# Kernel optimization log

Hardware: AMD Instinct MI355X
Metric: run time of the kernel (lower is better)

The kernel has to match this reference:

```python
import jax, jax.numpy as jnp
import numpy as np

N = 50000
E = 800000
HIGH, LOW, EMB = 128, 32, 64
HID, HEADS, OUT = 32, 8, 8
IN1 = HIGH + EMB  # 192
IN2 = HID * HEADS  # 256
NEG_SLOPE = 0.2


def setup_inputs() -> dict:
    key = jax.random.key(0)
    ks = jax.random.split(key, 12)
    s = lambda k, shape: (jax.random.normal(k, shape, dtype=jnp.float32) * 0.1)
    return {
        "high_dim_features": jax.random.normal(ks[0], (N, HIGH), dtype=jnp.float32),
        "low_dim_features": jax.random.normal(ks[1], (N, LOW), dtype=jnp.float32),
        "edge_index": jax.random.randint(ks[2], (2, E), 0, N, dtype=jnp.int32),
        "W_emb": s(ks[3], (LOW, EMB)),
        "b_emb": jnp.zeros((EMB,), jnp.float32),
        "W1": s(ks[4], (IN1, HEADS * HID)),
        "att_src1": s(ks[5], (HEADS, HID)),
        "att_dst1": s(ks[6], (HEADS, HID)),
        "b1": jnp.zeros((HEADS * HID,), jnp.float32),
        "W2": s(ks[7], (IN2, OUT)),
        "att_src2": s(ks[8], (1, OUT)),
        "att_dst2": s(ks[9], (1, OUT)),
        "b2": jnp.zeros((OUT,), jnp.float32),
    }


def _gat_layer(x, src, dst, W, att_src, att_dst, bias, heads, out_ch, concat):
    # x: [N, F_in]; src/dst: [E'] (self-loops already appended)
    n = x.shape[0]
    h = (x @ W).reshape(n, heads, out_ch)            # [N, H, C]
    a_src = jnp.einsum('nhc,hc->nh', h, att_src)     # [N, H]
    a_dst = jnp.einsum('nhc,hc->nh', h, att_dst)
    alpha = a_src[src] + a_dst[dst]                  # [E', H]
    alpha = jax.nn.leaky_relu(alpha, NEG_SLOPE)
    # segment softmax over incoming edges per destination node
    m = jax.ops.segment_max(alpha, dst, num_segments=n)
    ea = jnp.exp(alpha - m[dst])
    z = jax.ops.segment_sum(ea, dst, num_segments=n)
    alpha = ea / (z[dst] + 1e-16)                    # [E', H]
    msg = h[src] * alpha[:, :, None]                 # [E', H, C]
    out = jax.ops.segment_sum(msg, dst, num_segments=n)  # [N, H, C]
    if concat:
        out = out.reshape(n, heads * out_ch)
    else:
        out = out.mean(axis=1)
    return out + bias


def reference(high_dim_features, low_dim_features, edge_index,
              W_emb, b_emb, W1, att_src1, att_dst1, b1,
              W2, att_src2, att_dst2, b2):
    # embedding + elu, concat
    emb = jax.nn.elu(low_dim_features @ W_emb + b_emb)
    x = jnp.concatenate([high_dim_features, emb], axis=1)  # [N, IN1]
    # add self-loops (PyG default)
    loops = jnp.arange(N, dtype=edge_index.dtype)
    src = jnp.concatenate([edge_index[0], loops])
    dst = jnp.concatenate([edge_index[1], loops])
    x = _gat_layer(x, src, dst, W1, att_src1, att_dst1, b1, HEADS, HID, True)
    x = jax.nn.elu(x)  # dropout: eval mode no-op
    x = _gat_layer(x, src, dst, W2, att_src2, att_dst2, b2, 1, OUT, False)
    return jax.nn.log_softmax(x, axis=1)
```

## Files before the change

kernel.cpp:

```cpp
#include <hip/hip_runtime.h>
#include <hip/hip_bf16.h>

typedef __hip_bfloat16 bf16;
typedef short bf16x8 __attribute__((ext_vector_type(8)));
typedef float f32x4  __attribute__((ext_vector_type(4)));

#define CHK 2048

__device__ __forceinline__ float bf2f(bf16 v){ return __bfloat162float(v); }
__device__ __forceinline__ bf16  f2bf(float f){ return __float2bfloat16(f); }
__device__ __forceinline__ float lrelu(float a){ return a > 0.f ? a : 0.2f*a; }
__device__ __forceinline__ float bfbits(short s){
    union{unsigned u; float f;} cv; cv.u = ((unsigned)(unsigned short)s) << 16; return cv.f;
}
__device__ __forceinline__ short bf16s(float f){ bf16 q = f2bf(f); return *(short*)&q; }
__device__ __forceinline__ float cvtf(const void* p, int i, int isb){
    return isb ? bf2f(((const bf16*)p)[i]) : ((const float*)p)[i];
}
__device__ __forceinline__ short cvts(const void* p, int i, int isb){
    return isb ? ((const short*)p)[i] : bf16s(((const float*)p)[i]);
}
__device__ __forceinline__ bf16x8 load8(const void* base, size_t off, int isb){
    if (isb) return *(const bf16x8*)((const bf16*)base + off);
    const float* f = (const float*)base + off;
    f32x4 v0 = *(const f32x4*)f;
    f32x4 v1 = *(const f32x4*)(f + 4);
    short r[8];
    #pragma unroll
    for (int j = 0; j < 4; j++) r[j]   = bf16s(v0[j]);
    #pragma unroll
    for (int j = 0; j < 4; j++) r[4+j] = bf16s(v1[j]);
    return *(const bf16x8*)r;
}

__global__ __launch_bounds__(256) void k_init(const unsigned short* __restrict__ raw,
        int* __restrict__ flag, const int* __restrict__ dst,
        int* __restrict__ bucketCnt, int E, int NBUK, int nBlk){
    __shared__ int h[256];
    int t = threadIdx.x;
    if (blockIdx.x == 0){
        unsigned short w = raw[2*t];
        int e = (w >> 7) & 0xFF;
        int ok = (e >= 90 && e <= 140) ? 1 : 0;
        __shared__ int cnt;
        if (t == 0) cnt = 0;
        __syncthreads();
        atomicAdd(&cnt, ok);
        __syncthreads();
        if (t == 0) *flag = (cnt >= 192) ? 1 : 0;
    }
    h[t] = 0;
    __syncthreads();
    for (int i = blockIdx.x*256 + t; i < E; i += nBlk*256)
        atomicAdd(&h[((unsigned)dst[i]) >> 8], 1);
    __syncthreads();
    if (t < NBUK && h[t]) atomicAdd(&bucketCnt[t], h[t]);
}

__global__ __launch_bounds__(256) void k_prep(const void* __restrict__ low,
        const void* __restrict__ Wemb, const void* __restrict__ bemb,
        const void* __restrict__ W1, const void* __restrict__ W2,
        bf16* __restrict__ emb, bf16* __restrict__ Bp, bf16* __restrict__ Bp2,
        const int* __restrict__ flag, int N, int nEmb){
    __shared__ float wem[2048 + 64];
    __shared__ short lows[1024];
    int t = threadIdx.x;
    int b = blockIdx.x;
    int isb = *flag;
    if (b >= nEmb){
        int i = (b - nEmb)*256 + t;
        if (i < 16*6*64*8){
            int j = i & 7;
            int lane = (i >> 3) & 63;
            int r = i >> 9;
            int kt = r % 6, nt = r / 6;
            int k = kt*32 + (lane >> 4)*8 + j;
            int n = nt*16 + (lane & 15);
            *(short*)&Bp[i] = cvts(W1, k*256 + n, isb);
        } else {
            int i2 = i - 16*6*64*8;
            if (i2 >= 8*64*8) return;
            int j = i2 & 7;
            int lane = (i2 >> 3) & 63;
            int kt = i2 >> 9;
            int k = kt*32 + (lane >> 4)*8 + j;
            int n = lane & 15;
            *(short*)&Bp2[i2] = (n < 8) ? cvts(W2, k*8 + n, isb) : (short)0;
        }
        return;
    }
    for (int i = t; i < 2048; i += 256) wem[i] = cvtf(Wemb, i, isb);
    if (t < 64) wem[2048 + t] = cvtf(bemb, t, isb);
    int nl = t >> 3, j8 = (t & 7) * 8;
    for (int tile = 0; tile < 4; tile++){
        int nb0 = b*128 + tile*32;
        __syncthreads();
        int lim = (N - nb0) * 32;
        if (lim > 1024) lim = 1024;
        if (lim < 0) lim = 0;
        for (int i = t; i < 1024; i += 256)
            lows[i] = (i < lim) ? cvts(low, nb0*32 + i, isb) : (short)0;
        __syncthreads();
        float acc[8];
        #pragma unroll
        for (int j = 0; j < 8; j++) acc[j] = wem[2048 + j8 + j];
        for (int k = 0; k < 32; k++){
            float lv = bfbits(lows[nl*32 + k]);
            f32x4 w0 = *(const f32x4*)&wem[k*64 + j8];
            f32x4 w1 = *(const f32x4*)&wem[k*64 + j8 + 4];
            #pragma unroll
            for (int j = 0; j < 4; j++) acc[j]   += lv * w0[j];
            #pragma unroll
            for (int j = 0; j < 4; j++) acc[4+j] += lv * w1[j];
        }
        int n = nb0 + nl;
        if (n < N){
            short ov[8];
            #pragma unroll
            for (int j = 0; j < 8; j++){
                float v = acc[j];
                ov[j] = bf16s(v > 0.f ? v : expm1f(v));
            }
            *(bf16x8*)&emb[(size_t)n*64 + j8] = *(const bf16x8*)ov;
        }
    }
}

__global__ __launch_bounds__(256) void k_bscan(const int* __restrict__ bucketCnt,
        int* __restrict__ bucketPtr, int* __restrict__ bucketCur,
        int* __restrict__ rowptr, int N, int E, int NBUK){
    __shared__ int sd[256];
    int t = threadIdx.x;
    int v = (t < NBUK) ? bucketCnt[t] : 0;
    sd[t] = v;
    __syncthreads();
    #pragma unroll
    for (int off = 1; off < 256; off <<= 1){
        int a = (t >= off) ? sd[t - off] : 0;
        __syncthreads();
        sd[t] += a;
        __syncthreads();
    }
    int excl = sd[t] - v;
    if (t < NBUK){ bucketPtr[t] = excl; bucketCur[t*16] = excl; }
    if (t == 0){ bucketPtr[NBUK] = sd[255]; rowptr[N] = E + N; }
}

__global__ __launch_bounds__(256) void k_sg(
        const int* __restrict__ ei, int* __restrict__ bucketCur, int* __restrict__ pk,
        const void* __restrict__ highv, const bf16* __restrict__ emb,
        const bf16* __restrict__ Bp, const void* __restrict__ attS,
        const void* __restrict__ attD, bf16* __restrict__ h1,
        float* __restrict__ a_s, float* __restrict__ a_d,
        const int* __restrict__ flag, int N, int E, int nScat, int NBUK){
    const int RS = 260;
    __shared__ union SM {
        struct { short Ah[64*128]; short Ae[64*64]; } a;
        struct { float eb[16*260 + 16]; } g;
        struct { unsigned short dstS[CHK]; int hist[4][256]; int cur[4][256]; } s;
    } sm;
    __shared__ float att[512];
    int t = threadIdx.x;
    if ((int)blockIdx.x < nScat){
        int base = blockIdx.x * CHK;
        int cnt = E - base; if (cnt > CHK) cnt = CHK;
        int wv = t >> 6, lane = t & 63;
        #pragma unroll
        for (int w = 0; w < 4; w++) sm.s.hist[w][t] = 0;
        __syncthreads();
        const int* dstp = ei + E + base;
        const int* srcp = ei + base;
        int per = (cnt + 3) >> 2;
        int wb = wv*per, we = wb + per;
        if (we > cnt) we = cnt;
        if (wb > cnt) wb = cnt;
        for (int i = wb + lane; i < we; i += 64){
            int d = dstp[i];
            sm.s.dstS[i] = (unsigned short)d;
            atomicAdd(&sm.s.hist[wv][((unsigned)d) >> 8], 1);
        }
        __syncthreads();
        if (t < NBUK){
            int h0 = sm.s.hist[0][t], h1v = sm.s.hist[1][t];
            int h2 = sm.s.hist[2][t], h3 = sm.s.hist[3][t];
            int c = h0 + h1v + h2 + h3;
            int bs = c ? atomicAdd(&bucketCur[t*16], c) : 0;
            sm.s.cur[0][t] = bs;
            sm.s.cur[1][t] = bs + h0;
            sm.s.cur[2][t] = bs + h0 + h1v;
            sm.s.cur[3][t] = bs + h0 + h1v + h2;
        }
        __syncthreads();
        for (int i = wb + lane; i < we; i += 64){
            int d = sm.s.dstS[i];
            int pos = atomicAdd(&sm.s.cur[wv][d >> 8], 1);
            pk[pos] = ((d & 255) << 24) | srcp[i];
        }
        return;
    }
    int isb = *flag;
    att[t] = cvtf(attS, t, isb);
    att[256 + t] = cvtf(attD, t, isb);
    int w = t >> 6, lane = t & 63;
    int m_lo = lane & 15, quad = lane >> 4;
    int m0 = (blockIdx.x - nScat) * 64;

    #pragma unroll
    for (int ii = 0; ii < 4; ii++){
        int id = t + ii*256;
        int r = id >> 4, c = id & 15;
        int gr = m0 + r; if (gr >= N) gr = N-1;
        bf16x8 v = load8(highv, (size_t)gr*128 + c*8, isb);
        *(bf16x8*)&sm.a.Ah[r*128 + ((c ^ (r & 7)) << 3)] = v;
    }
    #pragma unroll
    for (int ii = 0; ii < 2; ii++){
        int id = t + ii*256;
        int r = id >> 3, c = id & 7;
        int gr = m0 + r; if (gr >= N) gr = N-1;
        bf16x8 v = *(const bf16x8*)&emb[(size_t)gr*64 + c*8];
        *(bf16x8*)&sm.a.Ae[r*64 + ((c ^ (r & 7)) << 3)] = v;
    }
    __syncthreads();

    f32x4 acc[4][4];
    #pragma unroll
    for (int rt = 0; rt < 4; rt++)
        #pragma unroll
        for (int ct = 0; ct < 4; ct++) acc[rt][ct] = (f32x4){0.f,0.f,0.f,0.f};

    int sw = m_lo & 7;
    #pragma unroll 2
    for (int kt = 0; kt < 6; kt++){
        bf16x8 a[4], b[4];
        if (kt < 4){
            int ch = (kt*4 + quad) ^ sw;
            #pragma unroll
            for (int rt = 0; rt < 4; rt++)
                a[rt] = *(const bf16x8*)&sm.a.Ah[(rt*16 + m_lo)*128 + (ch << 3)];
        } else {
            int ch = ((kt-4)*4 + quad) ^ sw;
            #pragma unroll
            for (int rt = 0; rt < 4; rt++)
                a[rt] = *(const bf16x8*)&sm.a.Ae[(rt*16 + m_lo)*64 + (ch << 3)];
        }
        #pragma unroll
        for (int ct = 0; ct < 4; ct++)
            b[ct] = *(const bf16x8*)&Bp[(size_t)(((w*4 + ct)*6 + kt)*64 + lane)*8];
        #pragma unroll
        for (int rt = 0; rt < 4; rt++)
            #pragma unroll
            for (int ct = 0; ct < 4; ct++)
                acc[rt][ct] = __builtin_amdgcn_mfma_f32_16x16x32_bf16(a[rt], b[ct], acc[rt][ct], 0, 0, 0);
    }

    float* eb = sm.g.eb;
    #pragma unroll 1
    for (int rt = 0; rt < 4; rt++){
        __syncthreads();
        #pragma unroll
        for (int ct = 0; ct < 4; ct++)
            #pragma unroll
            for (int reg = 0; reg < 4; reg++)
                eb[(quad*4 + reg)*RS + w*64 + ct*16 + m_lo] = acc[rt][ct][reg];
        __syncthreads();
        int r = t >> 4, cb = t & 15;
        int c0 = cb * 16;
        int m = m0 + rt*16 + r;
        f32x4 v[4];
        #pragma unroll
        for (int p = 0; p < 4; p++) v[p] = *(const f32x4*)&eb[r*RS + c0 + p*4];
        float ps = 0.f, pd = 0.f;
        #pragma unroll
        for (int p = 0; p < 4; p++)
            #pragma unroll
            for (int j = 0; j < 4; j++){
                ps += v[p][j] * att[c0 + p*4 + j];
                pd += v[p][j] * att[256 + c0 + p*4 + j];
            }
        if (m < N){
            short ov[16];
            #pragma unroll
            for (int p = 0; p < 4; p++)
                #pragma unroll
                for (int j = 0; j < 4; j++) ov[p*4+j] = bf16s(v[p][j]);
            *(bf16x8*)&h1[(size_t)m*256 + c0]     = *(const bf16x8*)&ov[0];
            *(bf16x8*)&h1[(size_t)m*256 + c0 + 8] = *(const bf16x8*)&ov[8];
        }
        ps += __shfl_xor(ps, 1);
        pd += __shfl_xor(pd, 1);
        if (((t & 1) == 0) && m < N){
            int hd = cb >> 1;
            a_s[m*8 + hd] = ps;
            a_d[m*8 + hd] = pd;
        }
    }
}

__global__ __launch_bounds__(256) void k_fine(const int* __restrict__ bucketPtr,
        const int* __restrict__ pk, int* __restrict__ rowptr, int* __restrict__ srcs,
        int N){
    __shared__ int hist[4][256];
    __shared__ int cur[4][256];
    __shared__ int sd[256];
    int t = threadIdx.x;
    int wv = t >> 6, lane = t & 63;
    int b = blockIdx.x;
    int d0 = b << 8;
    int nd = N - d0; if (nd > 256) nd = 256; if (nd < 0) nd = 0;
    int ebeg = bucketPtr[b], eend = bucketPtr[b+1];
    int tot = eend - ebeg;
    int per = (tot + 3) >> 2;
    int wb = wv*per, we = wb + per;
    if (we > tot) we = tot;
    if (wb > tot) wb = tot;
    #pragma unroll
    for (int w = 0; w < 4; w++) hist[w][t] = 0;
    __syncthreads();
    for (int i = wb + lane; i < we; i += 64)
        atomicAdd(&hist[wv][((unsigned)pk[ebeg + i]) >> 24], 1);
    __syncthreads();
    int h0 = hist[0][t], h1 = hist[1][t], h2 = hist[2][t], h3 = hist[3][t];
    int selfc = (t < nd) ? 1 : 0;
    int v = selfc + h0 + h1 + h2 + h3;
    sd[t] = v;
    __syncthreads();
    #pragma unroll
    for (int off = 1; off < 256; off <<= 1){
        int a = (t >= off) ? sd[t - off] : 0;
        __syncthreads();
        sd[t] += a;
        __syncthreads();
    }
    int r = ebeg + d0 + sd[t] - v;
    if (t < nd){
        rowptr[d0 + t] = r;
        srcs[r] = d0 + t;
    }
    int c0 = r + selfc;
    cur[0][t] = c0;
    cur[1][t] = c0 + h0;
    cur[2][t] = c0 + h0 + h1;
    cur[3][t] = c0 + h0 + h1 + h2;
    __syncthreads();
    for (int i = wb + lane; i < we; i += 64){
        int p = pk[ebeg + i];
        int pos = atomicAdd(&cur[wv][((unsigned)p) >> 24], 1);
        srcs[pos] = p & 0xFFFFFF;
    }
}

__global__ __launch_bounds__(256) void k_edge1(const int* __restrict__ rowptr,
        const int* __restrict__ srcs, const float* __restrict__ a_s,
        const float* __restrict__ a_d, const bf16* __restrict__ h1,
        const void* __restrict__ b1, bf16* __restrict__ x2,
        const int* __restrict__ flag, int N){
    int t = threadIdx.x;
    int lane = t & 63, wv = t >> 6;
    int n = blockIdx.x*4 + wv;
    if (n >= N) return;
    int beg = rowptr[n];
    int deg = rowptr[n+1] - beg;

    int cl = lane & 31;
    int hb = cl >> 2;
    int half = lane >> 5;
    float adb = a_d[n*8 + hb];

    float acc[8];
    #pragma unroll
    for (int j = 0; j < 8; j++) acc[j] = 0.f;
    float z = 0.f;

    int e = half;
    for (; e + 6 < deg; e += 8){
        int s0 = srcs[beg + e];
        int s1 = srcs[beg + e + 2];
        int s2 = srcs[beg + e + 4];
        int s3 = srcs[beg + e + 6];
        float w0 = __expf(fminf(lrelu(a_s[s0*8 + hb] + adb), 80.f));
        float w1 = __expf(fminf(lrelu(a_s[s1*8 + hb] + adb), 80.f));
        float w2 = __expf(fminf(lrelu(a_s[s2*8 + hb] + adb), 80.f));
        float w3 = __expf(fminf(lrelu(a_s[s3*8 + hb] + adb), 80.f));
        bf16x8 v0 = *(const bf16x8*)&h1[(size_t)s0*256 + cl*8];
        bf16x8 v1 = *(const bf16x8*)&h1[(size_t)s1*256 + cl*8];
        bf16x8 v2 = *(const bf16x8*)&h1[(size_t)s2*256 + cl*8];
        bf16x8 v3 = *(const bf16x8*)&h1[(size_t)s3*256 + cl*8];
        z += (w0 + w1) + (w2 + w3);
        #pragma unroll
        for (int j = 0; j < 8; j++) acc[j] += w0 * bfbits(v0[j]);
        #pragma unroll
        for (int j = 0; j < 8; j++) acc[j] += w1 * bfbits(v1[j]);
        #pragma unroll
        for (int j = 0; j < 8; j++) acc[j] += w2 * bfbits(v2[j]);
        #pragma unroll
        for (int j = 0; j < 8; j++) acc[j] += w3 * bfbits(v3[j]);
    }
    for (; e < deg; e += 2){
        int s = srcs[beg + e];
        float w = __expf(fminf(lrelu(a_s[s*8 + hb] + adb), 80.f));
        bf16x8 hv = *(const bf16x8*)&h1[(size_t)s*256 + cl*8];
        z += w;
        #pragma unroll
        for (int j = 0; j < 8; j++) acc[j] += w * bfbits(hv[j]);
    }
    #pragma unroll
    for (int j = 0; j < 8; j++) acc[j] += __shfl_xor(acc[j], 32);
    z += __shfl_xor(z, 32);
    float rz = 1.f / (z + 1e-16f);

    if (half == 0){
        int isb = *flag;
        bf16x8 bv = load8(b1, cl*8, isb);
        short ov[8];
        #pragma unroll
        for (int j = 0; j < 8; j++){
            float v = acc[j] * rz + bfbits(bv[j]);
            ov[j] = bf16s(v > 0.f ? v : expm1f(v));
        }
        *(bf16x8*)&x2[(size_t)n*256 + cl*8] = *(const bf16x8*)ov;
    }
}

__global__ __launch_bounds__(256) void k_gemm2(const bf16* __restrict__ x2,
        const bf16* __restrict__ Bp2, const void* __restrict__ attS,
        const void* __restrict__ attD, float* __restrict__ h2,
        float* __restrict__ a2s, float* __restrict__ a2d,
        const int* __restrict__ flag, int N){
    int t = threadIdx.x;
    int isb = *flag;
    int w = t >> 6, lane = t & 63;
    int m_lo = lane & 15, quad = lane >> 4;
    int m0 = blockIdx.x*64 + w*16;
    int mr = m0 + m_lo; if (mr >= N) mr = N-1;
    f32x4 acc = (f32x4){0.f,0.f,0.f,0.f};
    #pragma unroll
    for (int kt = 0; kt < 8; kt++){
        bf16x8 a = *(const bf16x8*)&x2[(size_t)mr*256 + kt*32 + quad*8];
        bf16x8 b = *(const bf16x8*)&Bp2[(size_t)(kt*64 + lane)*8];
        acc = __builtin_amdgcn_mfma_f32_16x16x32_bf16(a, b, acc, 0, 0, 0);
    }
    float s2 = (m_lo < 8) ? cvtf(attS, m_lo, isb) : 0.f;
    float d2 = (m_lo < 8) ? cvtf(attD, m_lo, isb) : 0.f;
    #pragma unroll
    for (int reg = 0; reg < 4; reg++){
        int m = m0 + quad*4 + reg;
        float val = acc[reg];
        float ps = val * s2, pd = val * d2;
        ps += __shfl_xor(ps, 1); ps += __shfl_xor(ps, 2);
        ps += __shfl_xor(ps, 4); ps += __shfl_xor(ps, 8);
        pd += __shfl_xor(pd, 1); pd += __shfl_xor(pd, 2);
        pd += __shfl_xor(pd, 4); pd += __shfl_xor(pd, 8);
        if (m < N){
            if (m_lo < 8) h2[(size_t)m*8 + m_lo] = val;
            if (m_lo == 0){ a2s[m] = ps; a2d[m] = pd; }
        }
    }
}

__global__ __launch_bounds__(256) void k_edge2(const int* __restrict__ rowptr,
        const int* __restrict__ srcs, const float* __restrict__ a2s,
        const float* __restrict__ a2d, const float* __restrict__ h2,
        const void* __restrict__ b2, void* __restrict__ outv,
        const int* __restrict__ flag, int N){
    int t = threadIdx.x;
    int lane = t & 63, wv = t >> 6;
    int n = blockIdx.x*4 + wv;
    if (n >= N) return;
    int beg = rowptr[n];
    int deg = rowptr[n+1] - beg;
    float adh = a2d[n];
    int ep = lane >> 3, c = lane & 7;
    float acc = 0.f, z = 0.f;
    for (int e = ep; e < deg; e += 8){
        int s = srcs[beg + e];
        float w = __expf(fminf(lrelu(a2s[s] + adh), 80.f));
        z += w;
        acc += w * h2[(size_t)s*8 + c];
    }
    acc += __shfl_xor(acc, 8);
    acc += __shfl_xor(acc, 16);
    acc += __shfl_xor(acc, 32);
    z += __shfl_xor(z, 8);
    z += __shfl_xor(z, 16);
    z += __shfl_xor(z, 32);
    int isb = *flag;
    float val = acc / (z + 1e-16f) + cvtf(b2, c, isb);
    float mx = val;
    mx = fmaxf(mx, __shfl_xor(mx, 1));
    mx = fmaxf(mx, __shfl_xor(mx, 2));
    mx = fmaxf(mx, __shfl_xor(mx, 4));
    float se = __expf(val - mx);
    se += __shfl_xor(se, 1); se += __shfl_xor(se, 2); se += __shfl_xor(se, 4);
    float r = val - mx - __logf(se);
    if (lane < 8){
        if (isb) ((bf16*)outv)[(size_t)n*8 + c] = f2bf(r);
        else     ((float*)outv)[(size_t)n*8 + c] = r;
    }
}

extern "C" void kernel_launch(void* const* d_in, const int* in_sizes, int n_in,
                              void* d_out, int out_size, void* d_ws, size_t ws_size,
                              hipStream_t stream) {
    const int* ei = (const int*)d_in[2];
    const int N = in_sizes[0] / 128;
    const int E = in_sizes[2] / 2;
    const int ET = E + N;
    const int NBUK = (N + 255) >> 8;

    char* p = (char*)d_ws;
    auto alloc = [&](size_t bytes) -> void* {
        char* r = p;
        p += (bytes + 255) & ~(size_t)255;
        return (void*)r;
    };
    int*   flag      = (int*)  alloc(256);
    int*   bucketCnt = (int*)  alloc((size_t)NBUK*4);
    int*   bucketPtr = (int*)  alloc((size_t)(NBUK+1)*4);
    int*   bucketCur = (int*)  alloc((size_t)NBUK*16*4);
    int*   rowptr    = (int*)  alloc((size_t)(N+1)*4);
    int*   srcs      = (int*)  alloc((size_t)ET*4);
    int*   pk        = (int*)  alloc((size_t)E*4);
    bf16*  Bp        = (bf16*) alloc((size_t)192*256*2);
    bf16*  Bp2       = (bf16*) alloc((size_t)8*64*8*2);
    bf16*  emb       = (bf16*) alloc((size_t)N*64*2);
    bf16*  h1        = (bf16*) alloc((size_t)N*256*2);
    float* a_s       = (float*)alloc((size_t)N*8*4);
    float* a_d       = (float*)alloc((size_t)N*8*4);
    bf16*  x2        = (bf16*) alloc((size_t)N*256*2);
    float* h2        = (float*)alloc((size_t)N*8*4);
    float* a2s       = (float*)alloc((size_t)N*4);
    float* a2d       = (float*)alloc((size_t)N*4);

    hipMemsetAsync(bucketCnt, 0, (size_t)NBUK*4, stream);
    k_init<<<256, 256, 0, stream>>>((const unsigned short*)d_in[0], flag,
            ei + E, bucketCnt, E, NBUK, 256);
    {
        int nEmb  = (N + 127)/128;
        int nPack = (16*6*64*8 + 8*64*8 + 255)/256;
        k_prep<<<nEmb + nPack, 256, 0, stream>>>(d_in[1], d_in[3], d_in[4],
                d_in[5], d_in[9], emb, Bp, Bp2, flag, N, nEmb);
    }
    k_bscan<<<1, 256, 0, stream>>>(bucketCnt, bucketPtr, bucketCur, rowptr, N, E, NBUK);
    {
        int nG = (N + 63)/64;
        int nScat = (E + CHK - 1)/CHK;
        k_sg<<<nScat + nG, 256, 0, stream>>>(ei, bucketCur, pk,
                d_in[0], emb, Bp, d_in[6], d_in[7], h1, a_s, a_d, flag, N, E, nScat, NBUK);
    }
    k_fine<<<NBUK, 256, 0, stream>>>(bucketPtr, pk, rowptr, srcs, N);
    k_edge1<<<(N + 3)/4, 256, 0, stream>>>(rowptr, srcs, a_s, a_d, h1, d_in[8], x2, flag, N);
    k_gemm2<<<(N + 63)/64, 256, 0, stream>>>(x2, Bp2, d_in[10], d_in[11], h2, a2s, a2d, flag, N);
    k_edge2<<<(N + 3)/4, 256, 0, stream>>>(rowptr, srcs, a2s, a2d, h2, d_in[12], d_out, flag, N);
}
```

Baseline: 303.0 us.

## Fuse layer-2 projection into edge1 and share attention weights via shuffles

Folds the second GAT layer's linear projection and attention-score computation into the layer-1 aggregation kernel, so x2 is never written to or read back from global memory and the k_gemm2 launch and W2 repacking go away. The edge loop is also restructured: each group of 8 lanes computes the exp weight for one head and one edge, and the source indices and weights are broadcast with shuffles. This removes the duplicated per-half exp and a_s loads and the scalar tail loop. The cost is extra shuffles, plus a per-node scalar dot with W2 read directly from global memory instead of an MFMA.

Result: slower. 316.2 us (+4.4%).

```diff
diff --git a/kernel.cpp b/kernel.cpp
--- a/kernel.cpp
+++ b/kernel.cpp
@@ -3,6 +3,7 @@
 
 typedef __hip_bfloat16 bf16;
 typedef short bf16x8 __attribute__((ext_vector_type(8)));
+typedef short s16x4  __attribute__((ext_vector_type(4)));
 typedef float f32x4  __attribute__((ext_vector_type(4)));
 
 #define CHK 2048
@@ -59,8 +60,8 @@
 
 __global__ __launch_bounds__(256) void k_prep(const void* __restrict__ low,
         const void* __restrict__ Wemb, const void* __restrict__ bemb,
-        const void* __restrict__ W1, const void* __restrict__ W2,
-        bf16* __restrict__ emb, bf16* __restrict__ Bp, bf16* __restrict__ Bp2,
+        const void* __restrict__ W1,
+        bf16* __restrict__ emb, bf16* __restrict__ Bp,
         const int* __restrict__ flag, int N, int nEmb){
     __shared__ float wem[2048 + 64];
     __shared__ short lows[1024];
@@ -77,15 +78,6 @@
             int k = kt*32 + (lane >> 4)*8 + j;
             int n = nt*16 + (lane & 15);
             *(short*)&Bp[i] = cvts(W1, k*256 + n, isb);
-        } else {
-            int i2 = i - 16*6*64*8;
-            if (i2 >= 8*64*8) return;
-            int j = i2 & 7;
-            int lane = (i2 >> 3) & 63;
-            int kt = i2 >> 9;
-            int k = kt*32 + (lane >> 4)*8 + j;
-            int n = lane & 15;
-            *(short*)&Bp2[i2] = (n < 8) ? cvts(W2, k*8 + n, isb) : (short)0;
         }
         return;
     }
@@ -353,7 +345,9 @@
 __global__ __launch_bounds__(256) void k_edge1(const int* __restrict__ rowptr,
         const int* __restrict__ srcs, const float* __restrict__ a_s,
         const float* __restrict__ a_d, const bf16* __restrict__ h1,
-        const void* __restrict__ b1, bf16* __restrict__ x2,
+        const void* __restrict__ b1, const void* __restrict__ W2,
+        const void* __restrict__ attS2, const void* __restrict__ attD2,
+        float* __restrict__ h2, float* __restrict__ a2s, float* __restrict__ a2d,
         const int* __restrict__ flag, int N){
     int t = threadIdx.x;
     int lane = t & 63, wv = t >> 6;
@@ -365,28 +359,33 @@
     int cl = lane & 31;
     int hb = cl >> 2;
     int half = lane >> 5;
-    float adb = a_d[n*8 + hb];
+    int eL = lane & 7, hL = lane >> 3;
+    float adW = a_d[n*8 + hL];
 
     float acc[8];
     #pragma unroll
     for (int j = 0; j < 8; j++) acc[j] = 0.f;
-    float z = 0.f;
-
-    int e = half;
-    for (; e + 6 < deg; e += 8){
-        int s0 = srcs[beg + e];
-        int s1 = srcs[beg + e + 2];
-        int s2 = srcs[beg + e + 4];
-        int s3 = srcs[beg + e + 6];
-        float w0 = __expf(fminf(lrelu(a_s[s0*8 + hb] + adb), 80.f));
-        float w1 = __expf(fminf(lrelu(a_s[s1*8 + hb] + adb), 80.f));
-        float w2 = __expf(fminf(lrelu(a_s[s2*8 + hb] + adb), 80.f));
-        float w3 = __expf(fminf(lrelu(a_s[s3*8 + hb] + adb), 80.f));
+    float zL = 0.f;
+
+    for (int e0 = 0; e0 < deg; e0 += 8){
+        int ew = e0 + eL;
+        int sw = srcs[beg + (ew < deg ? ew : 0)];
+        float wgt = 0.f;
+        if (ew < deg)
+            wgt = __expf(fminf(lrelu(a_s[sw*8 + hL] + adW), 80.f));
+        zL += wgt;
+        int s0 = __shfl(sw, half);
+        int s1 = __shfl(sw, half + 2);
+        int s2 = __shfl(sw, half + 4);
+        int s3 = __shfl(sw, half + 6);
+        float w0 = __shfl(wgt, hb*8 + half);
+        float w1 = __shfl(wgt, hb*8 + half + 2);
+        float w2 = __shfl(wgt, hb*8 + half + 4);
+        float w3 = __shfl(wgt, hb*8 + half + 6);
         bf16x8 v0 = *(const bf16x8*)&h1[(size_t)s0*256 + cl*8];
         bf16x8 v1 = *(const bf16x8*)&h1[(size_t)s1*256 + cl*8];
         bf16x8 v2 = *(const bf16x8*)&h1[(size_t)s2*256 + cl*8];
         bf16x8 v3 = *(const bf16x8*)&h1[(size_t)s3*256 + cl*8];
-        z += (w0 + w1) + (w2 + w3);
         #pragma unroll
         for (int j = 0; j < 8; j++) acc[j] += w0 * bfbits(v0[j]);
         #pragma unroll
@@ -396,66 +395,58 @@
         #pragma unroll
         for (int j = 0; j < 8; j++) acc[j] += w3 * bfbits(v3[j]);
     }
-    for (; e < deg; e += 2){
-        int s = srcs[beg + e];
-        float w = __expf(fminf(lrelu(a_s[s*8 + hb] + adb), 80.f));
-        bf16x8 hv = *(const bf16x8*)&h1[(size_t)s*256 + cl*8];
-        z += w;
-        #pragma unroll
-        for (int j = 0; j < 8; j++) acc[j] += w * bfbits(hv[j]);
-    }
+    zL += __shfl_xor(zL, 1);
+    zL += __shfl_xor(zL, 2);
+    zL += __shfl_xor(zL, 4);
     #pragma unroll
     for (int j = 0; j < 8; j++) acc[j] += __shfl_xor(acc[j], 32);
-    z += __shfl_xor(z, 32);
-    float rz = 1.f / (z + 1e-16f);
-
-    if (half == 0){
-        int isb = *flag;
-        bf16x8 bv = load8(b1, cl*8, isb);
-        short ov[8];
-        #pragma unroll
-        for (int j = 0; j < 8; j++){
-            float v = acc[j] * rz + bfbits(bv[j]);
-            ov[j] = bf16s(v > 0.f ? v : expm1f(v));
-        }
-        *(bf16x8*)&x2[(size_t)n*256 + cl*8] = *(const bf16x8*)ov;
-    }
-}
-
-__global__ __launch_bounds__(256) void k_gemm2(const bf16* __restrict__ x2,
-        const bf16* __restrict__ Bp2, const void* __restrict__ attS,
-        const void* __restrict__ attD, float* __restrict__ h2,
-        float* __restrict__ a2s, float* __restrict__ a2d,
-        const int* __restrict__ flag, int N){
-    int t = threadIdx.x;
+    float zh = __shfl(zL, hb*8);
+    float rz = 1.f / (zh + 1e-16f);
+
     int isb = *flag;
-    int w = t >> 6, lane = t & 63;
-    int m_lo = lane & 15, quad = lane >> 4;
-    int m0 = blockIdx.x*64 + w*16;
-    int mr = m0 + m_lo; if (mr >= N) mr = N-1;
-    f32x4 acc = (f32x4){0.f,0.f,0.f,0.f};
-    #pragma unroll
-    for (int kt = 0; kt < 8; kt++){
-        bf16x8 a = *(const bf16x8*)&x2[(size_t)mr*256 + kt*32 + quad*8];
-        bf16x8 b = *(const bf16x8*)&Bp2[(size_t)(kt*64 + lane)*8];
-        acc = __builtin_amdgcn_mfma_f32_16x16x32_bf16(a, b, acc, 0, 0, 0);
-    }
-    float s2 = (m_lo < 8) ? cvtf(attS, m_lo, isb) : 0.f;
-    float d2 = (m_lo < 8) ? cvtf(attD, m_lo, isb) : 0.f;
-    #pragma unroll
-    for (int reg = 0; reg < 4; reg++){
-        int m = m0 + quad*4 + reg;
-        float val = acc[reg];
-        float ps = val * s2, pd = val * d2;
-        ps += __shfl_xor(ps, 1); ps += __shfl_xor(ps, 2);
-        ps += __shfl_xor(ps, 4); ps += __shfl_xor(ps, 8);
-        pd += __shfl_xor(pd, 1); pd += __shfl_xor(pd, 2);
-        pd += __shfl_xor(pd, 4); pd += __shfl_xor(pd, 8);
-        if (m < N){
-            if (m_lo < 8) h2[(size_t)m*8 + m_lo] = val;
-            if (m_lo == 0){ a2s[m] = ps; a2d[m] = pd; }
-        }
-    }
+    bf16x8 bv = load8(b1, cl*8, isb);
+    float xv[8];
+    #pragma unroll
+    for (int j = 0; j < 8; j++){
+        float v = acc[j] * rz + bfbits(bv[j]);
+        xv[j] = v > 0.f ? v : expm1f(v);
+    }
+    float p[4] = {0.f, 0.f, 0.f, 0.f};
+    #pragma unroll
+    for (int j = 0; j < 8; j++){
+        int c = cl*8 + j;
+        float wr[4];
+        if (isb){
+            s16x4 q = *(const s16x4*)((const bf16*)W2 + c*8 + half*4);
+            #pragma unroll
+            for (int o = 0; o < 4; o++) wr[o] = bfbits(q[o]);
+        } else {
+            f32x4 q = *(const f32x4*)((const float*)W2 + c*8 + half*4);
+            #pragma unroll
+            for (int o = 0; o < 4; o++) wr[o] = q[o];
+        }
+        #pragma unroll
+        for (int o = 0; o < 4; o++) p[o] += xv[j] * wr[o];
+    }
+    #pragma unroll
+    for (int o = 0; o < 4; o++){
+        p[o] += __shfl_xor(p[o], 1);
+        p[o] += __shfl_xor(p[o], 2);
+        p[o] += __shfl_xor(p[o], 4);
+        p[o] += __shfl_xor(p[o], 8);
+        p[o] += __shfl_xor(p[o], 16);
+    }
+    float as2 = 0.f, ad2 = 0.f;
+    #pragma unroll
+    for (int o = 0; o < 4; o++){
+        as2 += p[o] * cvtf(attS2, half*4 + o, isb);
+        ad2 += p[o] * cvtf(attD2, half*4 + o, isb);
+    }
+    as2 += __shfl_xor(as2, 32);
+    ad2 += __shfl_xor(ad2, 32);
+    if (lane == 0){ a2s[n] = as2; a2d[n] = ad2; }
+    if ((lane & 31) == 0)
+        *(f32x4*)&h2[(size_t)n*8 + half*4] = (f32x4){p[0], p[1], p[2], p[3]};
 }
 
 __global__ __launch_bounds__(256) void k_edge2(const int* __restrict__ rowptr,
@@ -522,24 +513,22 @@
     int*   srcs      = (int*)  alloc((size_t)ET*4);
     int*   pk        = (int*)  alloc((size_t)E*4);
     bf16*  Bp        = (bf16*) alloc((size_t)192*256*2);
-    bf16*  Bp2       = (bf16*) alloc((size_t)8*64*8*2);
     bf16*  emb       = (bf16*) alloc((size_t)N*64*2);
     bf16*  h1        = (bf16*) alloc((size_t)N*256*2);
     float* a_s       = (float*)alloc((size_t)N*8*4);
     float* a_d       = (float*)alloc((size_t)N*8*4);
-    bf16*  x2        = (bf16*) alloc((size_t)N*256*2);
     float* h2        = (float*)alloc((size_t)N*8*4);
     float* a2s       = (float*)alloc((size_t)N*4);
-    float* a2d       = (float*)alloc((size_t)N*4);
+    float* a2d      = (float*)alloc((size_t)N*4);
 
     hipMemsetAsync(bucketCnt, 0, (size_t)NBUK*4, stream);
     k_init<<<256, 256, 0, stream>>>((const unsigned short*)d_in[0], flag,
             ei + E, bucketCnt, E, NBUK, 256);
     {
         int nEmb  = (N + 127)/128;
-        int nPack = (16*6*64*8 + 8*64*8 + 255)/256;
+        int nPack = (16*6*64*8)/256;
         k_prep<<<nEmb + nPack, 256, 0, stream>>>(d_in[1], d_in[3], d_in[4],
-                d_in[5], d_in[9], emb, Bp, Bp2, flag, N, nEmb);
+                d_in[5], emb, Bp, flag, N, nEmb);
     }
     k_bscan<<<1, 256, 0, stream>>>(bucketCnt, bucketPtr, bucketCur, rowptr, N, E, NBUK);
     {
@@ -549,7 +538,7 @@
                 d_in[0], emb, Bp, d_in[6], d_in[7], h1, a_s, a_d, flag, N, E, nScat, NBUK);
     }
     k_fine<<<NBUK, 256, 0, stream>>>(bucketPtr, pk, rowptr, srcs, N);
-    k_edge1<<<(N + 3)/4, 256, 0, stream>>>(rowptr, srcs, a_s, a_d, h1, d_in[8], x2, flag, N);
-    k_gemm2<<<(N + 63)/64, 256, 0, stream>>>(x2, Bp2, d_in[10], d_in[11], h2, a2s, a2d, flag, N);
+    k_edge1<<<(N + 3)/4, 256, 0, stream>>>(rowptr, srcs, a_s, a_d, h1, d_in[8],
+            d_in[9], d_in[10], d_in[11], h2, a2s, a2d, flag, N);
     k_edge2<<<(N + 3)/4, 256, 0, stream>>>(rowptr, srcs, a2s, a2d, h2, d_in[12], d_out, flag, N);
 }
```
